# Kernel optimization log

Measured on AMD Instinct MI355X. Metric: run time of the kernel, lower is better.

Reference implementation:

```python
import jax, jax.numpy as jnp
import numpy as np

B, LD, LQ, H = 16, 1024, 512, 1024


def setup_inputs() -> dict:
    key = jax.random.key(0)
    k1, k2, k3, k4 = jax.random.split(key, 4)
    D = jax.random.normal(k1, (B, LD, H), dtype=jnp.float32)
    Q = jax.random.normal(k2, (B, LQ, H), dtype=jnp.float32)
    # Padding-style masks derived from random valid lengths (True = masked).
    doc_lens = jax.random.randint(k3, (B,), 1, LD + 1, dtype=jnp.int32)
    q_lens = jax.random.randint(k4, (B,), 1, LQ + 1, dtype=jnp.int32)
    doc_mask = (jnp.arange(LD)[None, None, :] >= doc_lens[:, None, None])  # [B,1,LD]
    query_mask = (jnp.arange(LQ)[None, None, :] >= q_lens[:, None, None])  # [B,1,LQ]
    return {"D": D, "Q": Q, "doc_mask": doc_mask, "query_mask": query_mask,
            "doc_lens": doc_lens}


def reference(D, Q, doc_mask, query_mask, doc_lens):
    # Bidirectional cross-attention scores
    A_d = jnp.einsum('bdh,bqh->bdq', D, Q)          # [B,LD,LQ]
    A_q = jnp.einsum('bqh,bdh->bqd', Q, D)          # [B,LQ,LD]
    A_d = jax.nn.softmax(jnp.where(query_mask, -jnp.inf, A_d), axis=-1)
    A_q = jax.nn.softmax(jnp.where(doc_mask, -jnp.inf, A_q), axis=-1)
    C_q = jnp.einsum('bqd,bdh->bqh', A_q, D)        # [B,LQ,H]
    query_output = jnp.concatenate([Q, C_q], axis=-1)   # [B,LQ,2H]
    C_D = jnp.einsum('bdq,bqh->bdh', A_d, query_output)  # [B,LD,2H]
    doc_output = jnp.concatenate([C_D, D], axis=-1)      # [B,LD,3H]
    # extract_last: gather row at index (doc_lens - 1) along the seq dim
    idx = (doc_lens - 1).astype(jnp.int32)[:, None, None]  # [B,1,1]
    last = jnp.take_along_axis(doc_output, jnp.broadcast_to(idx, (doc_output.shape[0], 1, doc_output.shape[-1])), axis=1)
    last = jnp.squeeze(last, axis=1)                      # [B,3H]
    return doc_output, query_output, last
```

## Files before the change

kernel.cpp:

```cpp
#include <hip/hip_runtime.h>

#define B_   16
#define LD_  1024
#define LQ_  512
#define H_   1024

#define OUT0_F 0ull
#define OUT1_F 50331648ull
#define OUT2_F 67108864ull

#define OFF_DH   0ull
#define OFF_DL   33554432ull
#define OFF_QH   67108864ull
#define OFF_QL   83886080ull
#define OFF_S    100663296ull
#define OFF_AD   134217728ull
#define OFF_AQ   150994944ull
#define OFF_RM   167772160ull
#define OFF_RI   167837696ull
#define OFF_CPM  167903232ull
#define OFF_CPS  168427520ull
#define OFF_CM   168951808ull
#define OFF_CI   168984576ull
#define OFF_QLEN 169017344ull

typedef _Float16 half8 __attribute__((ext_vector_type(8)));
typedef _Float16 half4v __attribute__((ext_vector_type(4)));
typedef float floatx4 __attribute__((ext_vector_type(4)));

__device__ __forceinline__ void gll16(const _Float16* g, _Float16* l) {
#if __has_builtin(__builtin_amdgcn_global_load_lds)
  __builtin_amdgcn_global_load_lds(
      (const __attribute__((address_space(1))) unsigned int*)(unsigned long long)g,
      (__attribute__((address_space(3))) unsigned int*)(unsigned int)(unsigned long long)l,
      16, 0, 0);
#else
  int lane = threadIdx.x & 63;
  *(half8*)(l + lane * 8) = *(const half8*)(g + lane * 8);
#endif
}

__global__ void k_qlens(const unsigned char* qm, int* qlens) {
  __shared__ unsigned or_hi, is_f32;
  if (threadIdx.x == 0) { or_hi = 0u; is_f32 = 0u; }
  __syncthreads();
  const unsigned* w = (const unsigned*)qm;
  unsigned lo = 0u, lf = 0u;
  for (int i = threadIdx.x; i < (B_ * LQ_) / 4; i += 256) {
    unsigned v = w[i];
    lo |= (v >> 8);
    if (v == 0x3F800000u) lf = 1u;
  }
  atomicOr(&or_hi, lo);
  atomicOr(&is_f32, lf);
  __syncthreads();
  int esize4 = (or_hi == 0u) || is_f32;
  if (threadIdx.x < B_) {
    int b = threadIdx.x, cnt = 0;
    if (esize4) {
      const unsigned* p = (const unsigned*)qm + b * LQ_;
      for (int i = 0; i < LQ_; ++i) cnt += (p[i] == 0u);
    } else {
      const unsigned char* p = qm + b * LQ_;
      for (int i = 0; i < LQ_; ++i) cnt += (p[i] == 0);
    }
    qlens[b] = cnt;
  }
}

__global__ void k_cast(const float* __restrict__ Dp, const float* __restrict__ Qp,
                       _Float16* __restrict__ Dh, _Float16* __restrict__ Dl,
                       _Float16* __restrict__ Qh, _Float16* __restrict__ Ql,
                       float* __restrict__ out) {
  int t = blockIdx.x * 256 + threadIdx.x;
  const int nd4 = (B_ * LD_ * H_) / 4;
  const int nq4 = (B_ * LQ_ * H_) / 4;
  if (t < nd4) {
    float4 v = ((const float4*)Dp)[t];
    half4v hi, lo;
    hi[0] = (_Float16)v.x; lo[0] = (_Float16)(v.x - (float)hi[0]);
    hi[1] = (_Float16)v.y; lo[1] = (_Float16)(v.y - (float)hi[1]);
    hi[2] = (_Float16)v.z; lo[2] = (_Float16)(v.z - (float)hi[2]);
    hi[3] = (_Float16)v.w; lo[3] = (_Float16)(v.w - (float)hi[3]);
    ((half4v*)Dh)[t] = hi;
    ((half4v*)Dl)[t] = lo;
    int idx = t << 2, h = idx & (H_ - 1), bl = idx >> 10;
    *(float4*)(out + OUT0_F + (size_t)bl * 3072 + 2048 + h) = v;
  } else if (t < nd4 + nq4) {
    int u = t - nd4;
    float4 v = ((const float4*)Qp)[u];
    half4v hi, lo;
    hi[0] = (_Float16)v.x; lo[0] = (_Float16)(v.x - (float)hi[0]);
    hi[1] = (_Float16)v.y; lo[1] = (_Float16)(v.y - (float)hi[1]);
    hi[2] = (_Float16)v.z; lo[2] = (_Float16)(v.z - (float)hi[2]);
    hi[3] = (_Float16)v.w; lo[3] = (_Float16)(v.w - (float)hi[3]);
    ((half4v*)Qh)[u] = hi;
    ((half4v*)Ql)[u] = lo;
    int idx = u << 2, h = idx & (H_ - 1), bq = idx >> 10;
    *(float4*)(out + OUT1_F + (size_t)bq * 2048 + h) = v;
  }
}

__global__ __launch_bounds__(256) void k_gemm_scores(
    const _Float16* __restrict__ Dh, const _Float16* __restrict__ Dl,
    const _Float16* __restrict__ Qh, const _Float16* __restrict__ Ql,
    float* __restrict__ S) {
  int bid = blockIdx.x;
  int b = bid >> 5, t = bid & 31, tm = t >> 2, tn = t & 3;
  const int K = H_;
  const _Float16* Ah = Dh + (size_t)b * LD_ * H_;
  const _Float16* Al = Dl + (size_t)b * LD_ * H_;
  const _Float16* Bh = Qh + (size_t)b * LQ_ * H_;
  const _Float16* Bl = Ql + (size_t)b * LQ_ * H_;
  float* Cb = S + (size_t)b * LD_ * LQ_;

  __shared__ _Float16 sAh[128 * 32], sAl[128 * 32], sBh[128 * 32], sBl[128 * 32];
  int lane = threadIdx.x & 63, wave = threadIdx.x >> 6;
  int wm = wave >> 1, wn = wave & 1;
  int m0 = tm << 7, n0 = tn << 7;
  int srow = lane >> 2, scol = (lane & 3) << 3;

  floatx4 acc[4][4];
  floatx4 z = {0.f, 0.f, 0.f, 0.f};
#pragma unroll
  for (int i = 0; i < 4; ++i)
#pragma unroll
    for (int j = 0; j < 4; ++j) acc[i][j] = z;

  for (int k0 = 0; k0 < K; k0 += 32) {
#pragma unroll
    for (int ts = 0; ts < 2; ++ts) {
      int row = (wave << 5) + (ts << 4) + srow;
      int lo = ((wave << 5) + (ts << 4)) << 5;
      size_t ga = (size_t)(m0 + row) * K + k0 + scol;
      size_t gb = (size_t)(n0 + row) * K + k0 + scol;
      gll16(Ah + ga, sAh + lo);
      gll16(Al + ga, sAl + lo);
      gll16(Bh + gb, sBh + lo);
      gll16(Bl + gb, sBl + lo);
    }
    __syncthreads();
    int lk = (lane >> 4) << 3, lr = lane & 15;
    half8 ah[4], al4[4], bh[4], bl4[4];
#pragma unroll
    for (int i = 0; i < 4; ++i) {
      int ar = ((wm << 6) + (i << 4) + lr) << 5;
      int br = ((wn << 6) + (i << 4) + lr) << 5;
      ah[i]  = *(const half8*)(sAh + ar + lk);
      al4[i] = *(const half8*)(sAl + ar + lk);
      bh[i]  = *(const half8*)(sBh + br + lk);
      bl4[i] = *(const half8*)(sBl + br + lk);
    }
#pragma unroll
    for (int i = 0; i < 4; ++i)
#pragma unroll
      for (int j = 0; j < 4; ++j) {
        acc[i][j] = __builtin_amdgcn_mfma_f32_16x16x32_f16(ah[i],  bh[j],  acc[i][j], 0, 0, 0);
        acc[i][j] = __builtin_amdgcn_mfma_f32_16x16x32_f16(ah[i],  bl4[j], acc[i][j], 0, 0, 0);
        acc[i][j] = __builtin_amdgcn_mfma_f32_16x16x32_f16(al4[i], bh[j],  acc[i][j], 0, 0, 0);
      }
    __syncthreads();
  }
#pragma unroll
  for (int i = 0; i < 4; ++i) {
    int mb = m0 + (wm << 6) + (i << 4) + ((lane >> 4) << 2);
#pragma unroll
    for (int j = 0; j < 4; ++j) {
      int n = n0 + (wn << 6) + (j << 4) + (lane & 15);
#pragma unroll
      for (int rr = 0; rr < 4; ++rr)
        Cb[(size_t)(mb + rr) * LQ_ + n] = acc[i][j][rr];
    }
  }
}

__global__ void k_stats(const float* __restrict__ S, const int* qlens, const int* dlens,
                        float* rowmax, float* rowinv, float* colpM, float* colpS) {
  int b = blockIdx.x >> 4, ch = blockIdx.x & 15;
  int lane = threadIdx.x & 63, wave = threadIdx.x >> 6;
  int qlen = qlens[b], dlen = dlens[b];
  const float* Sb = S + (size_t)b * LD_ * LQ_;
  float cm[8], cs[8];
#pragma unroll
  for (int j = 0; j < 8; ++j) { cm[j] = -1e30f; cs[j] = 0.f; }
  for (int ri = 0; ri < 16; ++ri) {
    int d = (ch << 6) + (wave << 4) + ri;
    const float* row = Sb + (size_t)d * LQ_;
    float v[8], rm = -1e30f;
#pragma unroll
    for (int j = 0; j < 8; ++j) {
      int q = lane + (j << 6);
      v[j] = row[q];
      if (q < qlen) rm = fmaxf(rm, v[j]);
    }
    float rs = 0.f;
#pragma unroll
    for (int j = 0; j < 8; ++j) {
      int q = lane + (j << 6);
      if (q < qlen) rs += __expf(v[j] - rm);
    }
#pragma unroll
    for (int off = 32; off > 0; off >>= 1) {
      float om = __shfl_down(rm, off);
      float os = __shfl_down(rs, off);
      float nm = fmaxf(rm, om);
      rs = rs * __expf(rm - nm) + os * __expf(om - nm);
      rm = nm;
    }
    if (lane == 0) { rowmax[b * LD_ + d] = rm; rowinv[b * LD_ + d] = 1.0f / rs; }
    if (d < dlen) {
#pragma unroll
      for (int j = 0; j < 8; ++j) {
        float x = v[j];
        float nm = fmaxf(cm[j], x);
        cs[j] = cs[j] * __expf(cm[j] - nm) + __expf(x - nm);
        cm[j] = nm;
      }
    }
  }
  __shared__ float lm[4][512], ls[4][512];
#pragma unroll
  for (int j = 0; j < 8; ++j) {
    lm[wave][lane + (j << 6)] = cm[j];
    ls[wave][lane + (j << 6)] = cs[j];
  }
  __syncthreads();
  for (int q = threadIdx.x; q < 512; q += 256) {
    float m = lm[0][q], s = ls[0][q];
#pragma unroll
    for (int w = 1; w < 4; ++w) {
      float pm = lm[w][q], ps = ls[w][q];
      float nm = fmaxf(m, pm);
      s = s * __expf(m - nm) + ps * __expf(pm - nm);
      m = nm;
    }
    colpM[((b << 4) + ch) * LQ_ + q] = m;
    colpS[((b << 4) + ch) * LQ_ + q] = s;
  }
}

__global__ void k_colmerge(const float* colpM, const float* colpS,
                           float* colmax, float* colinv) {
  int t = blockIdx.x * 256 + threadIdx.x;
  int b = t >> 9, q = t & 511;
  float m = -1e30f, s = 0.f;
  for (int ch = 0; ch < 16; ++ch) {
    float pm = colpM[((b << 4) + ch) * LQ_ + q];
    float ps = colpS[((b << 4) + ch) * LQ_ + q];
    float nm = fmaxf(m, pm);
    s = s * __expf(m - nm) + ps * __expf(pm - nm);
    m = nm;
  }
  colmax[t] = m;
  colinv[t] = 1.0f / s;
}

__global__ void k_normalize(const float* __restrict__ S,
                            const float* rowmax, const float* rowinv,
                            const float* colmax, const float* colinv,
                            const int* qlens, const int* dlens,
                            _Float16* __restrict__ Ad, _Float16* __restrict__ Aq) {
  int blk = blockIdx.x;
  int b = blk >> 7, rest = blk & 127, dt = rest >> 3, qt = rest & 7;
  int d0 = dt << 6, q0 = qt << 6;
  int c = threadIdx.x & 63, w = threadIdx.x >> 6;
  int qlen = qlens[b], dlen = dlens[b];
  __shared__ _Float16 T[64 * 66];
  const float* Sb = S + (size_t)b * LD_ * LQ_;
  int q = q0 + c;
  float cmq = colmax[(b << 9) + q], ciq = colinv[(b << 9) + q];
  for (int i = 0; i < 16; ++i) {
    int r = (i << 2) + w, d = d0 + r;
    float s = Sb[(size_t)d * LQ_ + q];
    float ad = (q < qlen) ? __expf(s - rowmax[(b << 10) + d]) * rowinv[(b << 10) + d] : 0.f;
    Ad[(size_t)b * LD_ * LQ_ + (size_t)d * LQ_ + q] = (_Float16)ad;
    float aq = (d < dlen) ? __expf(s - cmq) * ciq : 0.f;
    T[c * 66 + r] = (_Float16)aq;
  }
  __syncthreads();
  for (int i = 0; i < 16; ++i) {
    int rq = (i << 2) + w;
    Aq[(size_t)b * LQ_ * LD_ + (size_t)(q0 + rq) * LD_ + d0 + c] = T[rq * 66 + c];
  }
}

__global__ void k_transpose(const _Float16* __restrict__ Dh, const _Float16* __restrict__ Qh,
                            _Float16* __restrict__ DhT, _Float16* __restrict__ QT) {
  int bid = blockIdx.x;
  const _Float16* src;
  _Float16* dst;
  int ld_out, r0, c0;
  if (bid < 4096) {
    int b = bid >> 8, t = bid & 255, tr = t >> 4, tc = t & 15;
    src = Dh + (size_t)b * LD_ * H_;
    dst = DhT + (size_t)b * H_ * LD_;
    ld_out = LD_; r0 = tr << 6; c0 = tc << 6;
  } else {
    int t2 = bid - 4096;
    int b = t2 >> 7, t = t2 & 127, tr = t >> 4, tc = t & 15;
    src = Qh + (size_t)b * LQ_ * H_;
    dst = QT + (size_t)b * 2 * H_ * LQ_;
    ld_out = LQ_; r0 = tr << 6; c0 = tc << 6;
  }
  int c = threadIdx.x & 63, w = threadIdx.x >> 6;
  __shared__ _Float16 T[64 * 66];
  for (int i = 0; i < 16; ++i) {
    int r = (i << 2) + w;
    T[c * 66 + r] = src[(size_t)(r0 + r) * H_ + c0 + c];
  }
  __syncthreads();
  for (int i = 0; i < 16; ++i) {
    int r = (i << 2) + w;
    dst[(size_t)(c0 + r) * ld_out + r0 + c] = T[r * 66 + c];
  }
}

__global__ __launch_bounds__(256) void k_gemm_cq(const _Float16* __restrict__ DhT,
                                                 const _Float16* __restrict__ Aq,
                                                 _Float16* __restrict__ QT,
                                                 float* __restrict__ out) {
  int bid = blockIdx.x;
  int b = bid >> 5, t = bid & 31, tm = t >> 2, tn = t & 3;
  const int K = LD_;
  const _Float16* A = DhT + (size_t)b * H_ * LD_;
  const _Float16* Bm = Aq + (size_t)b * LQ_ * LD_;
  __shared__ _Float16 sA[128 * 32], sB[128 * 32];
  int lane = threadIdx.x & 63, wave = threadIdx.x >> 6;
  int wm = wave >> 1, wn = wave & 1;
  int m0 = tm << 7, n0 = tn << 7;
  int srow = lane >> 2, scol = (lane & 3) << 3;

  floatx4 acc[4][4];
  floatx4 z = {0.f, 0.f, 0.f, 0.f};
#pragma unroll
  for (int i = 0; i < 4; ++i)
#pragma unroll
    for (int j = 0; j < 4; ++j) acc[i][j] = z;

  for (int k0 = 0; k0 < K; k0 += 32) {
#pragma unroll
    for (int ts = 0; ts < 2; ++ts) {
      int row = (wave << 5) + (ts << 4) + srow;
      int lo = ((wave << 5) + (ts << 4)) << 5;
      gll16(A + (size_t)(m0 + row) * K + k0 + scol, sA + lo);
      gll16(Bm + (size_t)(n0 + row) * K + k0 + scol, sB + lo);
    }
    __syncthreads();
    int lk = (lane >> 4) << 3, lr = lane & 15;
    half8 af[4], bf[4];
#pragma unroll
    for (int i = 0; i < 4; ++i) {
      af[i] = *(const half8*)(sA + (((wm << 6) + (i << 4) + lr) << 5) + lk);
      bf[i] = *(const half8*)(sB + (((wn << 6) + (i << 4) + lr) << 5) + lk);
    }
#pragma unroll
    for (int i = 0; i < 4; ++i)
#pragma unroll
      for (int j = 0; j < 4; ++j)
        acc[i][j] = __builtin_amdgcn_mfma_f32_16x16x32_f16(af[i], bf[j], acc[i][j], 0, 0, 0);
    __syncthreads();
  }
  float* qoutb = out + OUT1_F + (size_t)b * LQ_ * 2048;
  _Float16* qtb = QT + (size_t)b * 2048 * LQ_;
#pragma unroll
  for (int i = 0; i < 4; ++i) {
    int m = m0 + (wm << 6) + (i << 4) + ((lane >> 4) << 2);
#pragma unroll
    for (int j = 0; j < 4; ++j) {
      int n = n0 + (wn << 6) + (j << 4) + (lane & 15);
      float4 v;
      v.x = acc[i][j][0]; v.y = acc[i][j][1]; v.z = acc[i][j][2]; v.w = acc[i][j][3];
      *(float4*)(qoutb + (size_t)n * 2048 + 1024 + m) = v;
#pragma unroll
      for (int rr = 0; rr < 4; ++rr)
        qtb[(size_t)(1024 + m + rr) * LQ_ + n] = (_Float16)acc[i][j][rr];
    }
  }
}

__global__ __launch_bounds__(256) void k_gemm_cd(const _Float16* __restrict__ Ad,
                                                 const _Float16* __restrict__ QT,
                                                 float* __restrict__ out) {
  int bid = blockIdx.x;
  int b = bid >> 7, t = bid & 127, tm = t >> 4, tn = t & 15;
  const int K = LQ_;
  const _Float16* A = Ad + (size_t)b * LD_ * LQ_;
  const _Float16* Bm = QT + (size_t)b * 2048 * LQ_;
  __shared__ _Float16 sA[128 * 32], sB[128 * 32];
  int lane = threadIdx.x & 63, wave = threadIdx.x >> 6;
  int wm = wave >> 1, wn = wave & 1;
  int m0 = tm << 7, n0 = tn << 7;
  int srow = lane >> 2, scol = (lane & 3) << 3;

  floatx4 acc[4][4];
  floatx4 z = {0.f, 0.f, 0.f, 0.f};
#pragma unroll
  for (int i = 0; i < 4; ++i)
#pragma unroll
    for (int j = 0; j < 4; ++j) acc[i][j] = z;

  for (int k0 = 0; k0 < K; k0 += 32) {
#pragma unroll
    for (int ts = 0; ts < 2; ++ts) {
      int row = (wave << 5) + (ts << 4) + srow;
      int lo = ((wave << 5) + (ts << 4)) << 5;
      gll16(A + (size_t)(m0 + row) * K + k0 + scol, sA + lo);
      gll16(Bm + (size_t)(n0 + row) * K + k0 + scol, sB + lo);
    }
    __syncthreads();
    int lk = (lane >> 4) << 3, lr = lane & 15;
    half8 af[4], bf[4];
#pragma unroll
    for (int i = 0; i < 4; ++i) {
      af[i] = *(const half8*)(sA + (((wm << 6) + (i << 4) + lr) << 5) + lk);
      bf[i] = *(const half8*)(sB + (((wn << 6) + (i << 4) + lr) << 5) + lk);
    }
#pragma unroll
    for (int i = 0; i < 4; ++i)
#pragma unroll
      for (int j = 0; j < 4; ++j)
        acc[i][j] = __builtin_amdgcn_mfma_f32_16x16x32_f16(af[i], bf[j], acc[i][j], 0, 0, 0);
    __syncthreads();
  }
  float* db = out + OUT0_F + (size_t)b * LD_ * 3072;
#pragma unroll
  for (int i = 0; i < 4; ++i) {
    int mb = m0 + (wm << 6) + (i << 4) + ((lane >> 4) << 2);
#pragma unroll
    for (int j = 0; j < 4; ++j) {
      int n = n0 + (wn << 6) + (j << 4) + (lane & 15);
#pragma unroll
      for (int rr = 0; rr < 4; ++rr)
        db[(size_t)(mb + rr) * 3072 + n] = acc[i][j][rr];
    }
  }
}

__global__ void k_last(const int* dlens, float* __restrict__ out) {
  int t = blockIdx.x * 256 + threadIdx.x;
  int b = t / 3072, i = t % 3072;
  out[OUT2_F + t] = out[OUT0_F + (size_t)b * LD_ * 3072 + (size_t)(dlens[b] - 1) * 3072 + i];
}

extern "C" void kernel_launch(void* const* d_in, const int* in_sizes, int n_in,
                              void* d_out, int out_size, void* d_ws, size_t ws_size,
                              hipStream_t stream) {
  const float* Dp = (const float*)d_in[0];
  const float* Qp = (const float*)d_in[1];
  const unsigned char* qmask = (const unsigned char*)d_in[3];
  const int* dlens = (const int*)d_in[4];
  float* out = (float*)d_out;
  char* ws = (char*)d_ws;

  _Float16* Dh  = (_Float16*)(ws + OFF_DH);
  _Float16* Dl  = (_Float16*)(ws + OFF_DL);
  _Float16* Qh  = (_Float16*)(ws + OFF_QH);
  _Float16* Ql  = (_Float16*)(ws + OFF_QL);
  float*    S   = (float*)(ws + OFF_S);
  _Float16* Ad  = (_Float16*)(ws + OFF_AD);
  _Float16* Aq  = (_Float16*)(ws + OFF_AQ);
  float*    rm  = (float*)(ws + OFF_RM);
  float*    ri  = (float*)(ws + OFF_RI);
  float*    cpm = (float*)(ws + OFF_CPM);
  float*    cps = (float*)(ws + OFF_CPS);
  float*    cm  = (float*)(ws + OFF_CM);
  float*    ci  = (float*)(ws + OFF_CI);
  int*      ql  = (int*)(ws + OFF_QLEN);
  _Float16* DhT = (_Float16*)(ws + OFF_DL);
  _Float16* QT  = (_Float16*)(ws + OFF_S);

  k_qlens<<<1, 256, 0, stream>>>(qmask, ql);
  k_cast<<<24576, 256, 0, stream>>>(Dp, Qp, Dh, Dl, Qh, Ql, out);
  k_gemm_scores<<<512, 256, 0, stream>>>(Dh, Dl, Qh, Ql, S);
  k_stats<<<256, 256, 0, stream>>>(S, ql, dlens, rm, ri, cpm, cps);
  k_colmerge<<<32, 256, 0, stream>>>(cpm, cps, cm, ci);
  k_normalize<<<2048, 256, 0, stream>>>(S, rm, ri, cm, ci, ql, dlens, Ad, Aq);
  k_transpose<<<6144, 256, 0, stream>>>(Dh, Qh, DhT, QT);
  k_gemm_cq<<<512, 256, 0, stream>>>(DhT, Aq, QT, out);
  k_gemm_cd<<<2048, 256, 0, stream>>>(Ad, QT, out);
  k_last<<<192, 256, 0, stream>>>(dlens, out);
}
```

Baseline: 585.1 us.

## Fuse softmax stats into scores GEMM, transpose into cast, drop gather kernel

Row and column softmax partial max/sum are now computed in the scores GEMM epilogue from accumulators, which removes the separate stats pass that re-read the full score matrix. The cast kernel now also writes the transposed fp16 copies of D and Q, so the standalone transpose kernel is gone. The last-row gather is folded into the cast and C_D GEMM epilogues. Other changes: an XCD-aware block-to-batch mapping, a swapped operand order for the C_q GEMM, and a parallel qlen count. The costs are a larger workspace and heavier GEMM epilogues that use more registers and do shuffle reductions.

```diff
diff --git a/kernel.cpp b/kernel.cpp
--- a/kernel.cpp
+++ b/kernel.cpp
@@ -16,13 +16,17 @@
 #define OFF_S    100663296ull
 #define OFF_AD   134217728ull
 #define OFF_AQ   150994944ull
-#define OFF_RM   167772160ull
-#define OFF_RI   167837696ull
-#define OFF_CPM  167903232ull
-#define OFF_CPS  168427520ull
-#define OFF_CM   168951808ull
-#define OFF_CI   168984576ull
-#define OFF_QLEN 169017344ull
+#define OFF_DHT  167772160ull
+#define OFF_QT   201326592ull
+#define OFF_RM   234881024ull
+#define OFF_RI   234946560ull
+#define OFF_CM   235012096ull
+#define OFF_CI   235044864ull
+#define OFF_QLEN 235077632ull
+#define OFF_RPM  235077888ull
+#define OFF_RPS  235340032ull
+#define OFF_CPM  235602176ull
+#define OFF_CPS  235864320ull
 
 typedef _Float16 half8 __attribute__((ext_vector_type(8)));
 typedef _Float16 half4v __attribute__((ext_vector_type(4)));
@@ -40,9 +44,17 @@
 #endif
 }
 
+__device__ __forceinline__ void omerge(float& m, float& s, float pm, float ps) {
+  float nm = fmaxf(m, pm);
+  s = s * __expf(m - nm) + ps * __expf(pm - nm);
+  m = nm;
+}
+
 __global__ void k_qlens(const unsigned char* qm, int* qlens) {
   __shared__ unsigned or_hi, is_f32;
+  __shared__ int scnt[B_];
   if (threadIdx.x == 0) { or_hi = 0u; is_f32 = 0u; }
+  if (threadIdx.x < B_) scnt[threadIdx.x] = 0;
   __syncthreads();
   const unsigned* w = (const unsigned*)qm;
   unsigned lo = 0u, lf = 0u;
@@ -51,62 +63,118 @@
     lo |= (v >> 8);
     if (v == 0x3F800000u) lf = 1u;
   }
-  atomicOr(&or_hi, lo);
-  atomicOr(&is_f32, lf);
+  if (lo) atomicOr(&or_hi, 1u);
+  if (lf) atomicOr(&is_f32, 1u);
   __syncthreads();
   int esize4 = (or_hi == 0u) || is_f32;
-  if (threadIdx.x < B_) {
-    int b = threadIdx.x, cnt = 0;
-    if (esize4) {
-      const unsigned* p = (const unsigned*)qm + b * LQ_;
-      for (int i = 0; i < LQ_; ++i) cnt += (p[i] == 0u);
-    } else {
-      const unsigned char* p = qm + b * LQ_;
-      for (int i = 0; i < LQ_; ++i) cnt += (p[i] == 0);
-    }
-    qlens[b] = cnt;
-  }
-}
-
-__global__ void k_cast(const float* __restrict__ Dp, const float* __restrict__ Qp,
-                       _Float16* __restrict__ Dh, _Float16* __restrict__ Dl,
-                       _Float16* __restrict__ Qh, _Float16* __restrict__ Ql,
-                       float* __restrict__ out) {
-  int t = blockIdx.x * 256 + threadIdx.x;
-  const int nd4 = (B_ * LD_ * H_) / 4;
-  const int nq4 = (B_ * LQ_ * H_) / 4;
-  if (t < nd4) {
-    float4 v = ((const float4*)Dp)[t];
-    half4v hi, lo;
-    hi[0] = (_Float16)v.x; lo[0] = (_Float16)(v.x - (float)hi[0]);
-    hi[1] = (_Float16)v.y; lo[1] = (_Float16)(v.y - (float)hi[1]);
-    hi[2] = (_Float16)v.z; lo[2] = (_Float16)(v.z - (float)hi[2]);
-    hi[3] = (_Float16)v.w; lo[3] = (_Float16)(v.w - (float)hi[3]);
-    ((half4v*)Dh)[t] = hi;
-    ((half4v*)Dl)[t] = lo;
-    int idx = t << 2, h = idx & (H_ - 1), bl = idx >> 10;
-    *(float4*)(out + OUT0_F + (size_t)bl * 3072 + 2048 + h) = v;
-  } else if (t < nd4 + nq4) {
-    int u = t - nd4;
-    float4 v = ((const float4*)Qp)[u];
-    half4v hi, lo;
-    hi[0] = (_Float16)v.x; lo[0] = (_Float16)(v.x - (float)hi[0]);
-    hi[1] = (_Float16)v.y; lo[1] = (_Float16)(v.y - (float)hi[1]);
-    hi[2] = (_Float16)v.z; lo[2] = (_Float16)(v.z - (float)hi[2]);
-    hi[3] = (_Float16)v.w; lo[3] = (_Float16)(v.w - (float)hi[3]);
-    ((half4v*)Qh)[u] = hi;
-    ((half4v*)Ql)[u] = lo;
-    int idx = u << 2, h = idx & (H_ - 1), bq = idx >> 10;
-    *(float4*)(out + OUT1_F + (size_t)bq * 2048 + h) = v;
+  for (int idx = threadIdx.x; idx < B_ * LQ_; idx += 256) {
+    int b = idx >> 9;
+    int z;
+    if (esize4) z = (((const unsigned*)qm)[idx] == 0u);
+    else        z = (qm[idx] == 0);
+    if (z) atomicAdd(&scnt[b], 1);
+  }
+  __syncthreads();
+  if (threadIdx.x < B_) qlens[threadIdx.x] = scnt[threadIdx.x];
+}
+
+__global__ __launch_bounds__(256) void k_cast(
+    const float* __restrict__ Dp, const float* __restrict__ Qp,
+    const int* __restrict__ dlens,
+    _Float16* __restrict__ Dh, _Float16* __restrict__ Dl,
+    _Float16* __restrict__ Qh, _Float16* __restrict__ Ql,
+    _Float16* __restrict__ DhT, _Float16* __restrict__ QT,
+    float* __restrict__ out) {
+  __shared__ _Float16 T[64 * 66];
+  int bid = blockIdx.x;
+  int t = threadIdx.x;
+  int r = t >> 2, cb = (t & 3) << 4;
+  bool isD = bid < 4096;
+  int b, r0, c0;
+  const float* src;
+  if (isD) {
+    b = bid >> 8; int rest = bid & 255; r0 = (rest >> 4) << 6; c0 = (rest & 15) << 6;
+    src = Dp + (size_t)b * LD_ * H_;
+  } else {
+    int t2 = bid - 4096;
+    b = t2 >> 7; int rest = t2 & 127; r0 = (rest >> 4) << 6; c0 = (rest & 15) << 6;
+    src = Qp + (size_t)b * LQ_ * H_;
+  }
+  size_t eoff = (size_t)(r0 + r) * H_ + c0 + cb;
+  float4 v[4];
+#pragma unroll
+  for (int k = 0; k < 4; ++k) v[k] = *(const float4*)(src + eoff + (k << 2));
+  half4v hi4[4], lo4[4];
+#pragma unroll
+  for (int k = 0; k < 4; ++k) {
+    const float* f = (const float*)&v[k];
+#pragma unroll
+    for (int e = 0; e < 4; ++e) {
+      _Float16 h = (_Float16)f[e];
+      hi4[k][e] = h;
+      lo4[k][e] = (_Float16)(f[e] - (float)h);
+    }
+  }
+  if (isD) {
+    _Float16* dh = Dh + (size_t)b * LD_ * H_ + eoff;
+    _Float16* dl = Dl + (size_t)b * LD_ * H_ + eoff;
+    float* dob = out + OUT0_F + (size_t)b * LD_ * 3072 + (size_t)(r0 + r) * 3072 + 2048 + c0 + cb;
+#pragma unroll
+    for (int k = 0; k < 4; ++k) {
+      *(half4v*)(dh + (k << 2)) = hi4[k];
+      *(half4v*)(dl + (k << 2)) = lo4[k];
+      *(float4*)(dob + (k << 2)) = v[k];
+    }
+    if (r0 + r == dlens[b] - 1) {
+      float* o2 = out + OUT2_F + (size_t)b * 3072 + 2048 + c0 + cb;
+#pragma unroll
+      for (int k = 0; k < 4; ++k) *(float4*)(o2 + (k << 2)) = v[k];
+    }
+  } else {
+    _Float16* qh = Qh + (size_t)b * LQ_ * H_ + eoff;
+    _Float16* ql = Ql + (size_t)b * LQ_ * H_ + eoff;
+    float* qob = out + OUT1_F + (size_t)b * LQ_ * 2048 + (size_t)(r0 + r) * 2048 + c0 + cb;
+#pragma unroll
+    for (int k = 0; k < 4; ++k) {
+      *(half4v*)(qh + (k << 2)) = hi4[k];
+      *(half4v*)(ql + (k << 2)) = lo4[k];
+      *(float4*)(qob + (k << 2)) = v[k];
+    }
+  }
+#pragma unroll
+  for (int k = 0; k < 4; ++k)
+#pragma unroll
+    for (int e = 0; e < 4; ++e)
+      T[r * 66 + cb + (k << 2) + e] = hi4[k][e];
+  __syncthreads();
+  int ho = t >> 2, wb = (t & 3) << 4;
+  half4v o[4];
+#pragma unroll
+  for (int k = 0; k < 4; ++k)
+#pragma unroll
+    for (int e = 0; e < 4; ++e)
+      o[k][e] = T[(wb + (k << 2) + e) * 66 + ho];
+  if (isD) {
+    _Float16* dt = DhT + (size_t)b * H_ * LD_ + (size_t)(c0 + ho) * LD_ + r0 + wb;
+#pragma unroll
+    for (int k = 0; k < 4; ++k) *(half4v*)(dt + (k << 2)) = o[k];
+  } else {
+    _Float16* qt = QT + (size_t)b * 2048 * LQ_ + (size_t)(c0 + ho) * LQ_ + r0 + wb;
+#pragma unroll
+    for (int k = 0; k < 4; ++k) *(half4v*)(qt + (k << 2)) = o[k];
   }
 }
 
 __global__ __launch_bounds__(256) void k_gemm_scores(
     const _Float16* __restrict__ Dh, const _Float16* __restrict__ Dl,
     const _Float16* __restrict__ Qh, const _Float16* __restrict__ Ql,
-    float* __restrict__ S) {
-  int bid = blockIdx.x;
-  int b = bid >> 5, t = bid & 31, tm = t >> 2, tn = t & 3;
+    float* __restrict__ S, const int* __restrict__ qlens, const int* __restrict__ dlens,
+    float* __restrict__ rowPM, float* __restrict__ rowPS,
+    float* __restrict__ colPM, float* __restrict__ colPS) {
+  int raw = blockIdx.x;
+  int xcd = raw & 7, idx = raw >> 3;
+  int b = xcd + ((idx >> 5) << 3);
+  int t = idx & 31, tm = t >> 2, tn = t & 3;
   const int K = H_;
   const _Float16* Ah = Dh + (size_t)b * LD_ * H_;
   const _Float16* Al = Dl + (size_t)b * LD_ * H_;
@@ -161,98 +229,116 @@
       }
     __syncthreads();
   }
+  int quad = lane >> 4, l15 = lane & 15;
 #pragma unroll
   for (int i = 0; i < 4; ++i) {
-    int mb = m0 + (wm << 6) + (i << 4) + ((lane >> 4) << 2);
+    int mb = m0 + (wm << 6) + (i << 4) + (quad << 2);
 #pragma unroll
     for (int j = 0; j < 4; ++j) {
-      int n = n0 + (wn << 6) + (j << 4) + (lane & 15);
+      int n = n0 + (wn << 6) + (j << 4) + l15;
 #pragma unroll
       for (int rr = 0; rr < 4; ++rr)
         Cb[(size_t)(mb + rr) * LQ_ + n] = acc[i][j][rr];
     }
   }
-}
-
-__global__ void k_stats(const float* __restrict__ S, const int* qlens, const int* dlens,
-                        float* rowmax, float* rowinv, float* colpM, float* colpS) {
-  int b = blockIdx.x >> 4, ch = blockIdx.x & 15;
-  int lane = threadIdx.x & 63, wave = threadIdx.x >> 6;
   int qlen = qlens[b], dlen = dlens[b];
-  const float* Sb = S + (size_t)b * LD_ * LQ_;
-  float cm[8], cs[8];
-#pragma unroll
-  for (int j = 0; j < 8; ++j) { cm[j] = -1e30f; cs[j] = 0.f; }
-  for (int ri = 0; ri < 16; ++ri) {
-    int d = (ch << 6) + (wave << 4) + ri;
-    const float* row = Sb + (size_t)d * LQ_;
-    float v[8], rm = -1e30f;
-#pragma unroll
-    for (int j = 0; j < 8; ++j) {
-      int q = lane + (j << 6);
-      v[j] = row[q];
-      if (q < qlen) rm = fmaxf(rm, v[j]);
-    }
-    float rs = 0.f;
-#pragma unroll
-    for (int j = 0; j < 8; ++j) {
-      int q = lane + (j << 6);
-      if (q < qlen) rs += __expf(v[j] - rm);
-    }
-#pragma unroll
-    for (int off = 32; off > 0; off >>= 1) {
-      float om = __shfl_down(rm, off);
-      float os = __shfl_down(rs, off);
-      float nm = fmaxf(rm, om);
-      rs = rs * __expf(rm - nm) + os * __expf(om - nm);
-      rm = nm;
-    }
-    if (lane == 0) { rowmax[b * LD_ + d] = rm; rowinv[b * LD_ + d] = 1.0f / rs; }
-    if (d < dlen) {
-#pragma unroll
-      for (int j = 0; j < 8; ++j) {
-        float x = v[j];
-        float nm = fmaxf(cm[j], x);
-        cs[j] = cs[j] * __expf(cm[j] - nm) + __expf(x - nm);
-        cm[j] = nm;
-      }
-    }
-  }
-  __shared__ float lm[4][512], ls[4][512];
-#pragma unroll
-  for (int j = 0; j < 8; ++j) {
-    lm[wave][lane + (j << 6)] = cm[j];
-    ls[wave][lane + (j << 6)] = cs[j];
+  float* redM = (float*)sAh;
+  float* redS = (float*)sAl;
+  float* cdM  = (float*)sBh;
+  float* cdS  = (float*)sBl;
+#pragma unroll
+  for (int i = 0; i < 4; ++i) {
+#pragma unroll
+    for (int rr = 0; rr < 4; ++rr) {
+      float mx = -1e30f;
+#pragma unroll
+      for (int j = 0; j < 4; ++j) {
+        int q = n0 + (wn << 6) + (j << 4) + l15;
+        if (q < qlen) mx = fmaxf(mx, acc[i][j][rr]);
+      }
+      float s = 0.f;
+#pragma unroll
+      for (int j = 0; j < 4; ++j) {
+        int q = n0 + (wn << 6) + (j << 4) + l15;
+        if (q < qlen) s += __expf(acc[i][j][rr] - mx);
+      }
+#pragma unroll
+      for (int off = 1; off < 16; off <<= 1) {
+        float om = __shfl_xor(mx, off);
+        float os = __shfl_xor(s, off);
+        omerge(mx, s, om, os);
+      }
+      if (l15 == 0) {
+        int rl = (wm << 6) + (i << 4) + (quad << 2) + rr;
+        redM[(rl << 1) + wn] = mx;
+        redS[(rl << 1) + wn] = s;
+      }
+    }
+  }
+#pragma unroll
+  for (int j = 0; j < 4; ++j) {
+    float mx = -1e30f;
+#pragma unroll
+    for (int i = 0; i < 4; ++i)
+#pragma unroll
+      for (int rr = 0; rr < 4; ++rr) {
+        int d = m0 + (wm << 6) + (i << 4) + (quad << 2) + rr;
+        if (d < dlen) mx = fmaxf(mx, acc[i][j][rr]);
+      }
+    float s = 0.f;
+#pragma unroll
+    for (int i = 0; i < 4; ++i)
+#pragma unroll
+      for (int rr = 0; rr < 4; ++rr) {
+        int d = m0 + (wm << 6) + (i << 4) + (quad << 2) + rr;
+        if (d < dlen) s += __expf(acc[i][j][rr] - mx);
+      }
+#pragma unroll
+    for (int off = 16; off < 64; off <<= 1) {
+      float om = __shfl_xor(mx, off);
+      float os = __shfl_xor(s, off);
+      omerge(mx, s, om, os);
+    }
+    if (quad == 0) {
+      int cl = (wn << 6) + (j << 4) + l15;
+      cdM[(cl << 1) + wm] = mx;
+      cdS[(cl << 1) + wm] = s;
+    }
   }
   __syncthreads();
-  for (int q = threadIdx.x; q < 512; q += 256) {
-    float m = lm[0][q], s = ls[0][q];
-#pragma unroll
-    for (int w = 1; w < 4; ++w) {
-      float pm = lm[w][q], ps = ls[w][q];
-      float nm = fmaxf(m, pm);
-      s = s * __expf(m - nm) + ps * __expf(pm - nm);
-      m = nm;
-    }
-    colpM[((b << 4) + ch) * LQ_ + q] = m;
-    colpS[((b << 4) + ch) * LQ_ + q] = s;
-  }
-}
-
-__global__ void k_colmerge(const float* colpM, const float* colpS,
-                           float* colmax, float* colinv) {
+  if (threadIdx.x < 128) {
+    int rl = threadIdx.x;
+    float m1 = redM[rl << 1], s1 = redS[rl << 1];
+    omerge(m1, s1, redM[(rl << 1) + 1], redS[(rl << 1) + 1]);
+    int gr = b * LD_ + m0 + rl;
+    rowPM[tn * (B_ * LD_) + gr] = m1;
+    rowPS[tn * (B_ * LD_) + gr] = s1;
+  } else {
+    int cl = threadIdx.x - 128;
+    float m1 = cdM[cl << 1], s1 = cdS[cl << 1];
+    omerge(m1, s1, cdM[(cl << 1) + 1], cdS[(cl << 1) + 1]);
+    int gc = b * LQ_ + n0 + cl;
+    colPM[tm * (B_ * LQ_) + gc] = m1;
+    colPS[tm * (B_ * LQ_) + gc] = s1;
+  }
+}
+
+__global__ void k_merge(const float* __restrict__ rowPM, const float* __restrict__ rowPS,
+                        const float* __restrict__ colPM, const float* __restrict__ colPS,
+                        float* rm, float* ri, float* cm2, float* ci) {
   int t = blockIdx.x * 256 + threadIdx.x;
-  int b = t >> 9, q = t & 511;
-  float m = -1e30f, s = 0.f;
-  for (int ch = 0; ch < 16; ++ch) {
-    float pm = colpM[((b << 4) + ch) * LQ_ + q];
-    float ps = colpS[((b << 4) + ch) * LQ_ + q];
-    float nm = fmaxf(m, pm);
-    s = s * __expf(m - nm) + ps * __expf(pm - nm);
-    m = nm;
-  }
-  colmax[t] = m;
-  colinv[t] = 1.0f / s;
+  if (t < B_ * LD_) {
+    float m = -1e30f, s = 0.f;
+#pragma unroll
+    for (int c = 0; c < 4; ++c) omerge(m, s, rowPM[c * (B_ * LD_) + t], rowPS[c * (B_ * LD_) + t]);
+    rm[t] = m; ri[t] = 1.0f / s;
+  } else if (t < B_ * LD_ + B_ * LQ_) {
+    int u = t - B_ * LD_;
+    float m = -1e30f, s = 0.f;
+#pragma unroll
+    for (int c = 0; c < 8; ++c) omerge(m, s, colPM[c * (B_ * LQ_) + u], colPS[c * (B_ * LQ_) + u]);
+    cm2[u] = m; ci[u] = 1.0f / s;
+  }
 }
 
 __global__ void k_normalize(const float* __restrict__ S,
@@ -284,46 +370,17 @@
   }
 }
 
-__global__ void k_transpose(const _Float16* __restrict__ Dh, const _Float16* __restrict__ Qh,
-                            _Float16* __restrict__ DhT, _Float16* __restrict__ QT) {
-  int bid = blockIdx.x;
-  const _Float16* src;
-  _Float16* dst;
-  int ld_out, r0, c0;
-  if (bid < 4096) {
-    int b = bid >> 8, t = bid & 255, tr = t >> 4, tc = t & 15;
-    src = Dh + (size_t)b * LD_ * H_;
-    dst = DhT + (size_t)b * H_ * LD_;
-    ld_out = LD_; r0 = tr << 6; c0 = tc << 6;
-  } else {
-    int t2 = bid - 4096;
-    int b = t2 >> 7, t = t2 & 127, tr = t >> 4, tc = t & 15;
-    src = Qh + (size_t)b * LQ_ * H_;
-    dst = QT + (size_t)b * 2 * H_ * LQ_;
-    ld_out = LQ_; r0 = tr << 6; c0 = tc << 6;
-  }
-  int c = threadIdx.x & 63, w = threadIdx.x >> 6;
-  __shared__ _Float16 T[64 * 66];
-  for (int i = 0; i < 16; ++i) {
-    int r = (i << 2) + w;
-    T[c * 66 + r] = src[(size_t)(r0 + r) * H_ + c0 + c];
-  }
-  __syncthreads();
-  for (int i = 0; i < 16; ++i) {
-    int r = (i << 2) + w;
-    dst[(size_t)(c0 + r) * ld_out + r0 + c] = T[r * 66 + c];
-  }
-}
-
-__global__ __launch_bounds__(256) void k_gemm_cq(const _Float16* __restrict__ DhT,
-                                                 const _Float16* __restrict__ Aq,
+__global__ __launch_bounds__(256) void k_gemm_cq(const _Float16* __restrict__ Aq,
+                                                 const _Float16* __restrict__ DhT,
                                                  _Float16* __restrict__ QT,
                                                  float* __restrict__ out) {
-  int bid = blockIdx.x;
-  int b = bid >> 5, t = bid & 31, tm = t >> 2, tn = t & 3;
+  int raw = blockIdx.x;
+  int xcd = raw & 7, idx = raw >> 3;
+  int b = xcd + ((idx >> 5) << 3);
+  int t = idx & 31, tm = t >> 3, tn = t & 7;
   const int K = LD_;
-  const _Float16* A = DhT + (size_t)b * H_ * LD_;
-  const _Float16* Bm = Aq + (size_t)b * LQ_ * LD_;
+  const _Float16* A = Aq + (size_t)b * LQ_ * LD_;
+  const _Float16* Bm = DhT + (size_t)b * H_ * LD_;
   __shared__ _Float16 sA[128 * 32], sB[128 * 32];
   int lane = threadIdx.x & 63, wave = threadIdx.x >> 6;
   int wm = wave >> 1, wn = wave & 1;
@@ -362,27 +419,32 @@
   }
   float* qoutb = out + OUT1_F + (size_t)b * LQ_ * 2048;
   _Float16* qtb = QT + (size_t)b * 2048 * LQ_;
+  int quad = lane >> 4, l15 = lane & 15;
 #pragma unroll
   for (int i = 0; i < 4; ++i) {
-    int m = m0 + (wm << 6) + (i << 4) + ((lane >> 4) << 2);
+    int q = m0 + (wm << 6) + (i << 4) + (quad << 2);
 #pragma unroll
     for (int j = 0; j < 4; ++j) {
-      int n = n0 + (wn << 6) + (j << 4) + (lane & 15);
-      float4 v;
-      v.x = acc[i][j][0]; v.y = acc[i][j][1]; v.z = acc[i][j][2]; v.w = acc[i][j][3];
-      *(float4*)(qoutb + (size_t)n * 2048 + 1024 + m) = v;
+      int h = n0 + (wn << 6) + (j << 4) + l15;
 #pragma unroll
       for (int rr = 0; rr < 4; ++rr)
-        qtb[(size_t)(1024 + m + rr) * LQ_ + n] = (_Float16)acc[i][j][rr];
+        qoutb[(size_t)(q + rr) * 2048 + 1024 + h] = acc[i][j][rr];
+      half4v hv;
+#pragma unroll
+      for (int rr = 0; rr < 4; ++rr) hv[rr] = (_Float16)acc[i][j][rr];
+      *(half4v*)(qtb + (size_t)(1024 + h) * LQ_ + q) = hv;
     }
   }
 }
 
 __global__ __launch_bounds__(256) void k_gemm_cd(const _Float16* __restrict__ Ad,
                                                  const _Float16* __restrict__ QT,
+                                                 const int* __restrict__ dlens,
                                                  float* __restrict__ out) {
-  int bid = blockIdx.x;
-  int b = bid >> 7, t = bid & 127, tm = t >> 4, tn = t & 15;
+  int raw = blockIdx.x;
+  int xcd = raw & 7, idx = raw >> 3;
+  int b = xcd + ((idx >> 7) << 3);
+  int tile = idx & 127, tm = tile >> 4, tn = tile & 15;
   const int K = LQ_;
   const _Float16* A = Ad + (size_t)b * LD_ * LQ_;
   const _Float16* Bm = QT + (size_t)b * 2048 * LQ_;
@@ -423,23 +485,21 @@
     __syncthreads();
   }
   float* db = out + OUT0_F + (size_t)b * LD_ * 3072;
+  int dlast = dlens[b] - 1;
+  int quad = lane >> 4, l15 = lane & 15;
 #pragma unroll
   for (int i = 0; i < 4; ++i) {
-    int mb = m0 + (wm << 6) + (i << 4) + ((lane >> 4) << 2);
+    int mb = m0 + (wm << 6) + (i << 4) + (quad << 2);
 #pragma unroll
     for (int j = 0; j < 4; ++j) {
-      int n = n0 + (wn << 6) + (j << 4) + (lane & 15);
-#pragma unroll
-      for (int rr = 0; rr < 4; ++rr)
+      int n = n0 + (wn << 6) + (j << 4) + l15;
+#pragma unroll
+      for (int rr = 0; rr < 4; ++rr) {
         db[(size_t)(mb + rr) * 3072 + n] = acc[i][j][rr];
-    }
-  }
-}
-
-__global__ void k_last(const int* dlens, float* __restrict__ out) {
-  int t = blockIdx.x * 256 + threadIdx.x;
-  int b = t / 3072, i = t % 3072;
-  out[OUT2_F + t] = out[OUT0_F + (size_t)b * LD_ * 3072 + (size_t)(dlens[b] - 1) * 3072 + i];
+        if (mb + rr == dlast) out[OUT2_F + (size_t)b * 3072 + n] = acc[i][j][rr];
+      }
+    }
+  }
 }
 
 extern "C" void kernel_launch(void* const* d_in, const int* in_sizes, int n_in,
@@ -459,24 +519,23 @@
   float*    S   = (float*)(ws + OFF_S);
   _Float16* Ad  = (_Float16*)(ws + OFF_AD);
   _Float16* Aq  = (_Float16*)(ws + OFF_AQ);
+  _Float16* DhT = (_Float16*)(ws + OFF_DHT);
+  _Float16* QT  = (_Float16*)(ws + OFF_QT);
   float*    rm  = (float*)(ws + OFF_RM);
   float*    ri  = (float*)(ws + OFF_RI);
-  float*    cpm = (float*)(ws + OFF_CPM);
-  float*    cps = (float*)(ws + OFF_CPS);
   float*    cm  = (float*)(ws + OFF_CM);
   float*    ci  = (float*)(ws + OFF_CI);
   int*      ql  = (int*)(ws + OFF_QLEN);
-  _Float16* DhT = (_Float16*)(ws + OFF_DL);
-  _Float16* QT  = (_Float16*)(ws + OFF_S);
+  float*    rpm = (float*)(ws + OFF_RPM);
+  float*    rps = (float*)(ws + OFF_RPS);
+  float*    cpm = (float*)(ws + OFF_CPM);
+  float*    cps = (float*)(ws + OFF_CPS);
 
   k_qlens<<<1, 256, 0, stream>>>(qmask, ql);
-  k_cast<<<24576, 256, 0, stream>>>(Dp, Qp, Dh, Dl, Qh, Ql, out);
-  k_gemm_scores<<<512, 256, 0, stream>>>(Dh, Dl, Qh, Ql, S);
-  k_stats<<<256, 256, 0, stream>>>(S, ql, dlens, rm, ri, cpm, cps);
-  k_colmerge<<<32, 256, 0, stream>>>(cpm, cps, cm, ci);
+  k_cast<<<6144, 256, 0, stream>>>(Dp, Qp, dlens, Dh, Dl, Qh, Ql, DhT, QT, out);
+  k_gemm_scores<<<512, 256, 0, stream>>>(Dh, Dl, Qh, Ql, S, ql, dlens, rpm, rps, cpm, cps);
+  k_merge<<<96, 256, 0, stream>>>(rpm, rps, cpm, cps, rm, ri, cm, ci);
   k_normalize<<<2048, 256, 0, stream>>>(S, rm, ri, cm, ci, ql, dlens, Ad, Aq);
-  k_transpose<<<6144, 256, 0, stream>>>(Dh, Qh, DhT, QT);
-  k_gemm_cq<<<512, 256, 0, stream>>>(DhT, Aq, QT, out);
-  k_gemm_cd<<<2048, 256, 0, stream>>>(Ad, QT, out);
-  k_last<<<192, 256, 0, stream>>>(dlens, out);
-}
+  k_gemm_cq<<<512, 256, 0, stream>>>(Aq, DhT, QT, out);
+  k_gemm_cd<<<2048, 256, 0, stream>>>(Ad, QT, dlens, out);
+}
```

New measurement: 584.6 us. Within noise of the previous version (-0.1%).
